# Optimization experiments

Measured on AMD Instinct MI355X. Metric: run time of the kernel, lower is better.

## Reference

```python
import jax, jax.numpy as jnp
import numpy as np

N, TX, TZ, DX, DZ, DATT, DOUT = 8, 2048, 2048, 1024, 1024, 1024, 1024


def setup_inputs() -> dict:
    key = jax.random.key(0)
    ks = jax.random.split(key, 8)
    s = 0.02
    x = jax.random.normal(ks[0], (N, TX, DX), dtype=jnp.float32)
    z = jax.random.normal(ks[1], (N, TZ, DZ), dtype=jnp.float32)
    Wq = jax.random.normal(ks[2], (DX, DATT), dtype=jnp.float32) * s
    bq = jnp.zeros((DATT,), dtype=jnp.float32)
    Wk = jax.random.normal(ks[3], (DZ, DATT), dtype=jnp.float32) * s
    bk = jnp.zeros((DATT,), dtype=jnp.float32)
    Wv = jax.random.normal(ks[4], (DZ, DOUT), dtype=jnp.float32) * s
    bv = jnp.zeros((DOUT,), dtype=jnp.float32)
    # fixed boolean mask [Tx, Tz]; causal lower-triangular so no row is fully masked
    mask = jnp.tril(jnp.ones((TX, TZ), dtype=bool))
    return {"x": x, "z": z, "Wq": Wq, "bq": bq, "Wk": Wk, "bk": bk,
            "Wv": Wv, "bv": bv, "mask": mask}


def reference(x, z, Wq, bq, Wk, bk, Wv, bv, mask):
    Datt = Wq.shape[1]
    Q = x @ Wq + bq                      # [N, Tx, Datt]
    K = z @ Wk + bk                      # [N, Tz, Datt]
    V = z @ Wv + bv                      # [N, Tz, Dout]
    S = jnp.einsum('bxd,bzd->bxz', Q, K)  # [N, Tx, Tz]
    S = jnp.where(mask[None, :, :], S, -jnp.inf)
    A = jax.nn.softmax(S / jnp.sqrt(jnp.float32(Datt)), axis=-1)
    y = jnp.einsum('bxz,bzo->bxo', A, V)  # [N, Tx, Dout]
    return y
```

## Files before the change

kernel.cpp:

```cpp
#include <hip/hip_runtime.h>

typedef _Float16 f16;
typedef _Float16 f16x8 __attribute__((ext_vector_type(8)));
typedef _Float16 f16x4 __attribute__((ext_vector_type(4)));
typedef float    f32x4 __attribute__((ext_vector_type(4)));

constexpr int NB   = 8;
constexpr int T    = 2048;
constexpr int D    = 1024;
constexpr int SA_BATCH = 36 * 65536;

__device__ __forceinline__ void load_lds16(const f16* g, f16* l) {
    __builtin_amdgcn_global_load_lds(
        (const __attribute__((address_space(1))) void*)g,
        (__attribute__((address_space(3))) void*)l, 16, 0, 0);
}

__global__ __launch_bounds__(256) void cast_transpose_w(
    const float* __restrict__ W0, const float* __restrict__ W1,
    const float* __restrict__ W2, f16* __restrict__ Wt)
{
    __shared__ f16 tile[32][33];
    const int which = blockIdx.z;
    const float* W = which == 0 ? W0 : (which == 1 ? W1 : W2);
    f16* dst = Wt + (size_t)which * D * D;
    const int c0 = blockIdx.x * 32, r0 = blockIdx.y * 32;
    const int tx = threadIdx.x & 31, ty = threadIdx.x >> 5;
    #pragma unroll
    for (int i = 0; i < 32; i += 8)
        tile[ty + i][tx] = (f16)W[(size_t)(r0 + ty + i) * D + c0 + tx];
    __syncthreads();
    #pragma unroll
    for (int i = 0; i < 32; i += 8)
        dst[(size_t)(c0 + ty + i) * D + r0 + tx] = tile[tx][ty + i];
}

__global__ __launch_bounds__(256) void cast_xz(
    const float* __restrict__ x, const float* __restrict__ z,
    f16* __restrict__ xh, f16* __restrict__ zh)
{
    const float* src = blockIdx.y ? z : x;
    f16* dst = blockIdx.y ? zh : xh;
    const size_t i = ((size_t)blockIdx.x * 256 + threadIdx.x) * 4;
    const float4 v = *(const float4*)(src + i);
    f16x4 u = { (f16)v.x, (f16)v.y, (f16)v.z, (f16)v.w };
    *(f16x4*)(dst + i) = u;
}

template<int MODE>
__global__ __launch_bounds__(512, 2) void gemm_nt(
    const f16* __restrict__ Ag_, const f16* __restrict__ Bg_,
    void* __restrict__ Cg_, void* __restrict__ Cg2_,
    const float* __restrict__ bias, const float* __restrict__ bias2,
    float* __restrict__ rsum)
{
    __shared__ f16 As[2 * 256 * 64];
    __shared__ f16 Bs[2 * 256 * 64];

    int bx, by;
    const int bz = blockIdx.z;
    if (MODE == 1) {
        const int idx = blockIdx.x;
        by = (int)((sqrtf(8.0f * idx + 1.0f) - 1.0f) * 0.5f);
        while ((by + 1) * (by + 2) / 2 <= idx) ++by;
        while (by * (by + 1) / 2 > idx) --by;
        bx = idx - by * (by + 1) / 2;
    } else if (MODE == 2) {
        bx = blockIdx.x; by = 7 - blockIdx.y;
    } else {
        constexpr int GX  = (MODE == 0) ? 4 : 8;
        constexpr int LGX = (MODE == 0) ? 2 : 3;
        constexpr int NWG = GX * 64;
        int id = (int)blockIdx.y * GX + (int)blockIdx.x;
        id = (id & 7) * (NWG >> 3) + (id >> 3);
        bx = id & (GX - 1);
        by = id >> LGX;
    }

    const size_t bm0 = (size_t)by * 256, bn0 = (size_t)bx * 256;
    const f16* Abase; const f16* Bbase;
    int lda, ldb, K;
    if (MODE == 0 || MODE == 4) {
        Abase = Ag_ + bm0 * D;                       lda = D;
        Bbase = Bg_ + bn0 * D;                       ldb = D; K = D;
    } else if (MODE == 1) {
        Abase = Ag_ + (size_t)bz * T * D + bm0 * D;  lda = D;
        Bbase = Bg_ + (size_t)bz * T * D + bn0 * D;  ldb = D; K = D;
    } else {
        K = (by + 1) * 256; lda = K;
        Abase = Ag_ + (size_t)bz * SA_BATCH + (size_t)(by * (by + 1) / 2) * 65536;
        Bbase = Bg_ + (size_t)bz * D * T + bn0 * T;  ldb = T;
    }

    const int t    = threadIdx.x;
    const int lane = t & 63, wave = t >> 6;
    const int wr   = (wave >> 2) * 128, wc = (wave & 3) * 64;
    const int fr   = lane & 15, ho = lane >> 4;
    const int srow = t >> 3;
    const int scol = ((t & 7) ^ ((t >> 3) & 7)) * 8;
    const int wub  = wave * 512;
    const f16* Ap = Abase + (size_t)srow * lda + scol;
    const f16* Bp = Bbase + (size_t)srow * ldb + scol;
    const int fsw = fr & 7;

    f32x4 acc[8][4] = {};
    const int nk = K >> 6;

    auto stage = [&](int s, int b) {
        const size_t k = (size_t)s * 64;
        #pragma unroll
        for (int i = 0; i < 4; ++i)
            load_lds16(Ap + k + (size_t)(i * 64) * lda,
                       As + b * 16384 + i * 4096 + wub);
        #pragma unroll
        for (int i = 0; i < 4; ++i)
            load_lds16(Bp + k + (size_t)(i * 64) * ldb,
                       Bs + b * 16384 + i * 4096 + wub);
    };

    stage(0, 0);

    for (int s = 0; s < nk; ++s) {
        const int cur = s & 1;
        if (s + 1 < nk) {
            stage(s + 1, cur ^ 1);
            asm volatile("s_waitcnt vmcnt(8)" ::: "memory");
        } else {
            asm volatile("s_waitcnt vmcnt(0)" ::: "memory");
        }
        __builtin_amdgcn_sched_barrier(0);
        __builtin_amdgcn_s_barrier();
        __builtin_amdgcn_sched_barrier(0);

        const f16* Ab = As + cur * 16384;
        const f16* Bb = Bs + cur * 16384;
        #pragma unroll
        for (int kc = 0; kc < 2; ++kc) {
            const int ch = (((kc << 2) | ho) ^ fsw) << 3;
            f16x8 av[8], bv[4];
            #pragma unroll
            for (int i = 0; i < 8; ++i)
                av[i] = *(const f16x8*)&Ab[((wr + i * 16 + fr) << 6) + ch];
            #pragma unroll
            for (int j = 0; j < 4; ++j)
                bv[j] = *(const f16x8*)&Bb[((wc + j * 16 + fr) << 6) + ch];
            __builtin_amdgcn_s_setprio(1);
            #pragma unroll
            for (int i = 0; i < 8; ++i)
                #pragma unroll
                for (int j = 0; j < 4; ++j)
                    acc[i][j] = __builtin_amdgcn_mfma_f32_16x16x32_f16(av[i], bv[j], acc[i][j], 0, 0, 0);
            __builtin_amdgcn_s_setprio(0);
        }
        __builtin_amdgcn_sched_barrier(0);
        __builtin_amdgcn_s_barrier();
    }

    const int cr = (lane >> 4) * 4, cc = lane & 15;
    if (MODE == 0) {
        f16* Cp = (f16*)Cg_;
        #pragma unroll
        for (int j = 0; j < 4; ++j) {
            const int col = (int)bn0 + wc + j * 16 + cc;
            const float bb = bias[col];
            #pragma unroll
            for (int i = 0; i < 8; ++i)
                #pragma unroll
                for (int g = 0; g < 4; ++g)
                    Cp[(bm0 + wr + i * 16 + cr + g) * D + col] = (f16)(acc[i][j][g] + bb);
        }
    } else if (MODE == 4) {
        if (bx < 4) {
            f16* Cp = (f16*)Cg_;
            #pragma unroll
            for (int j = 0; j < 4; ++j) {
                const int col = (int)bn0 + wc + j * 16 + cc;
                const float bb = bias[col];
                #pragma unroll
                for (int i = 0; i < 8; ++i)
                    #pragma unroll
                    for (int g = 0; g < 4; ++g)
                        Cp[(bm0 + wr + i * 16 + cr + g) * D + col] = (f16)(acc[i][j][g] + bb);
            }
        } else {
            f16* Vt = (f16*)Cg2_;
            const int b  = (int)(bm0 >> 11);
            const int r0 = (int)(bm0 & 2047);
            #pragma unroll
            for (int j = 0; j < 4; ++j) {
                const int colv = (int)bn0 - 1024 + wc + j * 16 + cc;
                const float bb = bias2[colv];
                #pragma unroll
                for (int i = 0; i < 8; ++i) {
                    f16x4 pk = { (f16)(acc[i][j][0] + bb), (f16)(acc[i][j][1] + bb),
                                 (f16)(acc[i][j][2] + bb), (f16)(acc[i][j][3] + bb) };
                    *(f16x4*)&Vt[(size_t)b * D * T + (size_t)colv * T + r0 + wr + i * 16 + cr] = pk;
                }
            }
        }
    } else if (MODE == 1) {
        const int ldab = (by + 1) * 256;
        f16* Cp = (f16*)Cg_ + (size_t)bz * SA_BATCH
                + (size_t)(by * (by + 1) / 2) * 65536 + bn0;
        float* rs = rsum + (size_t)bz * T + bm0;
        #pragma unroll
        for (int i = 0; i < 8; ++i) {
            float rowsum[4] = {};
            #pragma unroll
            for (int j = 0; j < 4; ++j)
                #pragma unroll
                for (int g = 0; g < 4; ++g) {
                    const int lr = wr + i * 16 + cr + g, lc = wc + j * 16 + cc;
                    const int r = (int)bm0 + lr, c = (int)bn0 + lc;
                    const float p = (c > r) ? 0.0f : __expf(acc[i][j][g] * 0.03125f);
                    Cp[(size_t)lr * ldab + lc] = (f16)p;
                    rowsum[g] += p;
                }
            #pragma unroll
            for (int g = 0; g < 4; ++g) {
                float sv = rowsum[g];
                sv += __shfl_xor(sv, 1, 64);
                sv += __shfl_xor(sv, 2, 64);
                sv += __shfl_xor(sv, 4, 64);
                sv += __shfl_xor(sv, 8, 64);
                if (cc == 0) atomicAdd(&rs[wr + i * 16 + cr + g], sv);
            }
        }
    } else {
        float* Cp = (float*)Cg_ + (size_t)bz * T * D;
        const float* rs = rsum + (size_t)bz * T;
        #pragma unroll
        for (int i = 0; i < 8; ++i) {
            const int r4 = (int)bm0 + wr + i * 16 + cr;
            float rinv[4];
            #pragma unroll
            for (int g = 0; g < 4; ++g) rinv[g] = 1.0f / rs[r4 + g];
            #pragma unroll
            for (int j = 0; j < 4; ++j)
                #pragma unroll
                for (int g = 0; g < 4; ++g)
                    Cp[(size_t)(r4 + g) * D + bn0 + wc + j * 16 + cc] = acc[i][j][g] * rinv[g];
        }
    }
}

extern "C" void kernel_launch(void* const* d_in, const int* in_sizes, int n_in,
                              void* d_out, int out_size, void* d_ws, size_t ws_size,
                              hipStream_t stream)
{
    const float* x  = (const float*)d_in[0];
    const float* z  = (const float*)d_in[1];
    const float* Wq = (const float*)d_in[2];
    const float* bq = (const float*)d_in[3];
    const float* Wk = (const float*)d_in[4];
    const float* bk = (const float*)d_in[5];
    const float* Wv = (const float*)d_in[6];
    const float* bv = (const float*)d_in[7];
    float* out = (float*)d_out;

    char* ws = (char*)d_ws;
    f16*   Wt   = (f16*)(ws);
    f16*   xh   = (f16*)(ws + 6291456ull);
    f16*   zh   = (f16*)(ws + 39845888ull);
    f16*   Qh   = (f16*)(ws + 73400320ull);
    f16*   Kh   = (f16*)(ws + 106954752ull);
    f16*   Vt   = (f16*)(ws + 140509184ull);
    f16*   SA   = (f16*)(ws + 6291456ull);
    float* rsum = (float*)(ws + 209715200ull);

    hipMemsetAsync(rsum, 0, (size_t)NB * T * sizeof(float), stream);
    cast_transpose_w<<<dim3(32, 32, 3), 256, 0, stream>>>(Wq, Wk, Wv, Wt);
    cast_xz<<<dim3(16384, 2, 1), 256, 0, stream>>>(x, z, xh, zh);
    gemm_nt<0><<<dim3(4, 64, 1), 512, 0, stream>>>(xh, Wt, Qh, nullptr, bq, nullptr, nullptr);
    gemm_nt<4><<<dim3(8, 64, 1), 512, 0, stream>>>(zh, Wt + 1048576, Kh, Vt, bk, bv, nullptr);
    gemm_nt<1><<<dim3(36, 1, 8), 512, 0, stream>>>(Qh, Kh, SA, nullptr, nullptr, nullptr, rsum);
    gemm_nt<2><<<dim3(4, 8, 8), 512, 0, stream>>>(SA, Vt, out, nullptr, nullptr, nullptr, rsum);
}
```

Measured before the change: 463.5 us.

## Halve M-tile to 128 for QK^T and PV kernels and interleave batches

The score (MODE 1) and PV (MODE 2) GEMMs switch to 128-row M tiles. The triangular block enumeration is rewritten for half-height row blocks, and the batch index is folded into blockIdx.x so consecutive workgroups span different batches. This roughly doubles the workgroup count, 288 to 576 and 256 to 512, for better CU occupancy and load balance on the causal triangle. The cost is more redundant B-tile loads per output and a lower MFMA-to-load ratio per stage.

```diff
diff --git a/kernel.cpp b/kernel.cpp
--- a/kernel.cpp
+++ b/kernel.cpp
@@ -54,19 +54,26 @@
     const float* __restrict__ bias, const float* __restrict__ bias2,
     float* __restrict__ rsum)
 {
-    __shared__ f16 As[2 * 256 * 64];
+    constexpr int BM     = (MODE == 1 || MODE == 2) ? 128 : 256;
+    constexpr int MR     = BM / 32;
+    constexpr int ALOADS = BM / 64;
+    constexpr int SLOADS = ALOADS + 4;
+
+    __shared__ f16 As[2 * BM * 64];
     __shared__ f16 Bs[2 * 256 * 64];
 
-    int bx, by;
-    const int bz = blockIdx.z;
+    int bx, by, bz = blockIdx.z;
     if (MODE == 1) {
-        const int idx = blockIdx.x;
-        by = (int)((sqrtf(8.0f * idx + 1.0f) - 1.0f) * 0.5f);
-        while ((by + 1) * (by + 2) / 2 <= idx) ++by;
-        while (by * (by + 1) / 2 > idx) --by;
-        bx = idx - by * (by + 1) / 2;
+        const int p = blockIdx.x;
+        bz = p & 7;
+        const int u = p >> 3;
+        int cnt = 1, acc0 = 0; by = 0;
+        while (acc0 + cnt <= u) { acc0 += cnt; ++by; cnt = (by >> 1) + 1; }
+        bx = u - acc0;
     } else if (MODE == 2) {
-        bx = blockIdx.x; by = 7 - blockIdx.y;
+        const int xx = blockIdx.x;
+        bz = xx & 7; bx = xx >> 3;
+        by = 15 - (int)blockIdx.y;
     } else {
         constexpr int GX  = (MODE == 0) ? 4 : 8;
         constexpr int LGX = (MODE == 0) ? 2 : 3;
@@ -77,7 +84,7 @@
         by = id >> LGX;
     }
 
-    const size_t bm0 = (size_t)by * 256, bn0 = (size_t)bx * 256;
+    const size_t bm0 = (size_t)by * BM, bn0 = (size_t)bx * 256;
     const f16* Abase; const f16* Bbase;
     int lda, ldb, K;
     if (MODE == 0 || MODE == 4) {
@@ -87,14 +94,16 @@
         Abase = Ag_ + (size_t)bz * T * D + bm0 * D;  lda = D;
         Bbase = Bg_ + (size_t)bz * T * D + bn0 * D;  ldb = D; K = D;
     } else {
-        K = (by + 1) * 256; lda = K;
-        Abase = Ag_ + (size_t)bz * SA_BATCH + (size_t)(by * (by + 1) / 2) * 65536;
+        const int by2 = by >> 1;
+        K = (by2 + 1) * 256; lda = K;
+        Abase = Ag_ + (size_t)bz * SA_BATCH + (size_t)(by2 * (by2 + 1) / 2) * 65536
+              + (size_t)((by & 1) * 128) * K;
         Bbase = Bg_ + (size_t)bz * D * T + bn0 * T;  ldb = T;
     }
 
     const int t    = threadIdx.x;
     const int lane = t & 63, wave = t >> 6;
-    const int wr   = (wave >> 2) * 128, wc = (wave & 3) * 64;
+    const int wr   = (wave >> 2) * (BM / 2), wc = (wave & 3) * 64;
     const int fr   = lane & 15, ho = lane >> 4;
     const int srow = t >> 3;
     const int scol = ((t & 7) ^ ((t >> 3) & 7)) * 8;
@@ -103,15 +112,15 @@
     const f16* Bp = Bbase + (size_t)srow * ldb + scol;
     const int fsw = fr & 7;
 
-    f32x4 acc[8][4] = {};
+    f32x4 acc[MR][4] = {};
     const int nk = K >> 6;
 
     auto stage = [&](int s, int b) {
         const size_t k = (size_t)s * 64;
         #pragma unroll
-        for (int i = 0; i < 4; ++i)
+        for (int i = 0; i < ALOADS; ++i)
             load_lds16(Ap + k + (size_t)(i * 64) * lda,
-                       As + b * 16384 + i * 4096 + wub);
+                       As + b * (BM * 64) + i * 4096 + wub);
         #pragma unroll
         for (int i = 0; i < 4; ++i)
             load_lds16(Bp + k + (size_t)(i * 64) * ldb,
@@ -124,7 +133,10 @@
         const int cur = s & 1;
         if (s + 1 < nk) {
             stage(s + 1, cur ^ 1);
-            asm volatile("s_waitcnt vmcnt(8)" ::: "memory");
+            if constexpr (SLOADS == 8)
+                asm volatile("s_waitcnt vmcnt(8)" ::: "memory");
+            else
+                asm volatile("s_waitcnt vmcnt(6)" ::: "memory");
         } else {
             asm volatile("s_waitcnt vmcnt(0)" ::: "memory");
         }
@@ -132,21 +144,21 @@
         __builtin_amdgcn_s_barrier();
         __builtin_amdgcn_sched_barrier(0);
 
-        const f16* Ab = As + cur * 16384;
+        const f16* Ab = As + cur * (BM * 64);
         const f16* Bb = Bs + cur * 16384;
         #pragma unroll
         for (int kc = 0; kc < 2; ++kc) {
             const int ch = (((kc << 2) | ho) ^ fsw) << 3;
-            f16x8 av[8], bv[4];
-            #pragma unroll
-            for (int i = 0; i < 8; ++i)
+            f16x8 av[MR], bv[4];
+            #pragma unroll
+            for (int i = 0; i < MR; ++i)
                 av[i] = *(const f16x8*)&Ab[((wr + i * 16 + fr) << 6) + ch];
             #pragma unroll
             for (int j = 0; j < 4; ++j)
                 bv[j] = *(const f16x8*)&Bb[((wc + j * 16 + fr) << 6) + ch];
             __builtin_amdgcn_s_setprio(1);
             #pragma unroll
-            for (int i = 0; i < 8; ++i)
+            for (int i = 0; i < MR; ++i)
                 #pragma unroll
                 for (int j = 0; j < 4; ++j)
                     acc[i][j] = __builtin_amdgcn_mfma_f32_16x16x32_f16(av[i], bv[j], acc[i][j], 0, 0, 0);
@@ -164,7 +176,7 @@
             const int col = (int)bn0 + wc + j * 16 + cc;
             const float bb = bias[col];
             #pragma unroll
-            for (int i = 0; i < 8; ++i)
+            for (int i = 0; i < MR; ++i)
                 #pragma unroll
                 for (int g = 0; g < 4; ++g)
                     Cp[(bm0 + wr + i * 16 + cr + g) * D + col] = (f16)(acc[i][j][g] + bb);
@@ -177,7 +189,7 @@
                 const int col = (int)bn0 + wc + j * 16 + cc;
                 const float bb = bias[col];
                 #pragma unroll
-                for (int i = 0; i < 8; ++i)
+                for (int i = 0; i < MR; ++i)
                     #pragma unroll
                     for (int g = 0; g < 4; ++g)
                         Cp[(bm0 + wr + i * 16 + cr + g) * D + col] = (f16)(acc[i][j][g] + bb);
@@ -191,7 +203,7 @@
                 const int colv = (int)bn0 - 1024 + wc + j * 16 + cc;
                 const float bb = bias2[colv];
                 #pragma unroll
-                for (int i = 0; i < 8; ++i) {
+                for (int i = 0; i < MR; ++i) {
                     f16x4 pk = { (f16)(acc[i][j][0] + bb), (f16)(acc[i][j][1] + bb),
                                  (f16)(acc[i][j][2] + bb), (f16)(acc[i][j][3] + bb) };
                     *(f16x4*)&Vt[(size_t)b * D * T + (size_t)colv * T + r0 + wr + i * 16 + cr] = pk;
@@ -199,12 +211,14 @@
             }
         }
     } else if (MODE == 1) {
-        const int ldab = (by + 1) * 256;
+        const int by2  = by >> 1;
+        const int ldab = (by2 + 1) * 256;
         f16* Cp = (f16*)Cg_ + (size_t)bz * SA_BATCH
-                + (size_t)(by * (by + 1) / 2) * 65536 + bn0;
+                + (size_t)(by2 * (by2 + 1) / 2) * 65536
+                + (size_t)((by & 1) * 128) * ldab + bn0;
         float* rs = rsum + (size_t)bz * T + bm0;
         #pragma unroll
-        for (int i = 0; i < 8; ++i) {
+        for (int i = 0; i < MR; ++i) {
             float rowsum[4] = {};
             #pragma unroll
             for (int j = 0; j < 4; ++j)
@@ -230,7 +244,7 @@
         float* Cp = (float*)Cg_ + (size_t)bz * T * D;
         const float* rs = rsum + (size_t)bz * T;
         #pragma unroll
-        for (int i = 0; i < 8; ++i) {
+        for (int i = 0; i < MR; ++i) {
             const int r4 = (int)bm0 + wr + i * 16 + cr;
             float rinv[4];
             #pragma unroll
@@ -273,6 +287,6 @@
     cast_xz<<<dim3(16384, 2, 1), 256, 0, stream>>>(x, z, xh, zh);
     gemm_nt<0><<<dim3(4, 64, 1), 512, 0, stream>>>(xh, Wt, Qh, nullptr, bq, nullptr, nullptr);
     gemm_nt<4><<<dim3(8, 64, 1), 512, 0, stream>>>(zh, Wt + 1048576, Kh, Vt, bk, bv, nullptr);
-    gemm_nt<1><<<dim3(36, 1, 8), 512, 0, stream>>>(Qh, Kh, SA, nullptr, nullptr, nullptr, rsum);
-    gemm_nt<2><<<dim3(4, 8, 8), 512, 0, stream>>>(SA, Vt, out, nullptr, nullptr, nullptr, rsum);
-}
+    gemm_nt<1><<<dim3(576, 1, 1), 512, 0, stream>>>(Qh, Kh, SA, nullptr, nullptr, nullptr, rsum);
+    gemm_nt<2><<<dim3(32, 16, 1), 512, 0, stream>>>(SA, Vt, out, nullptr, nullptr, nullptr, rsum);
+}
```

After: 442.8 us. 4.5% less time.
